# Kernel tuning notes

Hardware: AMD Instinct MI355X
Metric: run time of the kernel (lower is better)

## Reference

```python
import jax, jax.numpy as jnp
import numpy as np

B, L, D, H = 4, 4096, 1024, 4
DK = D // H          # per-head dim, d_k == d_v == 256
C = 64               # chunk size for chunked delta rule
NC = L // C
KS = 4               # short-conv kernel size
EPS = 1e-5           # norm_eps


def _silu(x):
    return x * jax.nn.sigmoid(x)


def _l2norm(x):
    return x * jax.lax.rsqrt((x * x).sum(-1, keepdims=True) + 1e-6)


def _depthwise_conv(x, w):
    # x: [b, l, d], w: [d, ks]. torch Conv1d(groups=d, padding=ks//2) then trim to l
    # == asymmetric padding (ks//2, ks//2 - 1) giving exactly length l.
    xt = jnp.swapaxes(x, 1, 2)  # [b, d, l]
    out = jax.lax.conv_general_dilated(
        xt, w[:, None, :], window_strides=(1,), padding=[(KS // 2, KS // 2 - 1)],
        feature_group_count=x.shape[-1], dimension_numbers=('NCH', 'OIH', 'NCH'))
    return jnp.swapaxes(out, 1, 2)


def setup_inputs() -> dict:
    key = jax.random.key(0)
    ks = jax.random.split(key, 16)
    nrm = lambda k, shp, s: jax.random.normal(k, shp, jnp.float32) * s
    s = 0.02
    FH = DK // 2
    return {
        'x': nrm(ks[0], (B, L, D), 1.0),
        'Wq': nrm(ks[1], (D, D), s), 'Wk': nrm(ks[2], (D, D), s), 'Wv': nrm(ks[3], (D, D), s),
        'Wb': nrm(ks[4], (D, H), s), 'Wg': nrm(ks[5], (D, D), s), 'Wo': nrm(ks[6], (D, D), s),
        'cq': nrm(ks[7], (D, KS), 0.2), 'ck': nrm(ks[8], (D, KS), 0.2), 'cv': nrm(ks[9], (D, KS), 0.2),
        'Wbil': nrm(ks[10], (H, DK, DK), 0.1 / np.sqrt(DK)),
        'temp': jnp.full((H,), float(np.sqrt(DK)), jnp.float32),
        'fw1': nrm(ks[11], (2 * DK + 1, FH), s), 'fb1': jnp.zeros((FH,), jnp.float32),
        'fw2': nrm(ks[12], (FH, 1), s), 'fb2': jnp.zeros((1,), jnp.float32),
        'rms_w': jnp.ones((DK,), jnp.float32),
        'lam_fast': jnp.full((H,), 0.3, jnp.float32),
        'lam_slow': jnp.full((H,), 0.9, jnp.float32),
    }


def reference(x, Wq, Wk, Wv, Wb, Wg, Wo, cq, ck, cv, Wbil, temp,
              fw1, fb1, fw2, fb2, rms_w, lam_fast, lam_slow):
    b, l, d = x.shape
    h, dk = H, DK

    # projections + depthwise short convolution + silu (qk_activation='silu')
    q = _silu(_depthwise_conv(x @ Wq, cq))
    k = _silu(_depthwise_conv(x @ Wk, ck))
    v = _silu(_depthwise_conv(x @ Wv, cv))
    beta = jax.nn.sigmoid(x @ Wb)                      # [b, l, h]

    def to_chunks(t):
        # [b, l, h*dk] -> [b, h, nc, C, dk]
        return t.reshape(b, NC, C, h, dk).transpose(0, 3, 1, 2, 4)

    q = _l2norm(to_chunks(q))                          # qk_norm='l2'
    k = _l2norm(to_chunks(k))
    v = to_chunks(v)
    beta = beta.reshape(b, NC, C, h).transpose(0, 3, 1, 2)  # [b,h,nc,C]

    k_beta = k * beta[..., None]
    v_beta = v * beta[..., None]

    strict = jnp.tril(jnp.ones((C, C), x.dtype), -1)
    causal = jnp.tril(jnp.ones((C, C), x.dtype))

    # intra-chunk delta-rule solve: T = (I + strictly_lower(k_beta k^T))^-1
    A = jnp.einsum('bhncd,bhned->bhnce', k_beta, k) * strict
    T = jnp.linalg.inv(jnp.eye(C, dtype=x.dtype) + A)
    w = jnp.einsum('bhnce,bhned->bhncd', T, k_beta)    # [b,h,nc,C,dk]
    u = jnp.einsum('bhnce,bhned->bhncd', T, v_beta)    # [b,h,nc,C,dv]

    # chunk-level bilinear resonance flux (vectorized 5-dim branch)
    k_proj = jnp.einsum('bhnck,hkv->bhncv', k, Wbil)
    avg_attn = (k_proj * u).sum(-1).mean(-1) / temp[None, :, None]   # [b,h,nc]
    flux_in = jnp.concatenate([k.mean(3), u.mean(3), avg_attn[..., None]], -1)
    h1 = _silu(flux_in @ fw1 + fb1)
    psi = jnp.clip(jax.nn.sigmoid(h1 @ fw2 + fb2)[..., 0], 0.01, 0.99)  # [b,h,nc]

    # chunk-sequential scan with hierarchical dual-state memory
    qs = jnp.moveaxis(q, 2, 0)
    ks_ = jnp.moveaxis(k, 2, 0)
    ws = jnp.moveaxis(w, 2, 0)
    us = jnp.moveaxis(u, 2, 0)
    psis = jnp.moveaxis(psi, 2, 0)                     # [nc,b,h]
    S0 = jnp.zeros((b, h, dk, dk), x.dtype)
    lf = lam_fast[None, :, None, None]
    ls = lam_slow[None, :, None, None]

    def step(carry, inp):
        Sf, Ss = carry
        qc, kc, wc, uc, pc = inp
        S = Sf + Ss
        u_i = uc - jnp.einsum('bhcd,bhdv->bhcv', wc, S)
        attn = jnp.einsum('bhcd,bhed->bhce', qc, kc) * causal
        o = jnp.einsum('bhcd,bhdv->bhcv', qc, S) + jnp.einsum('bhce,bhev->bhcv', attn, u_i)
        dS = jnp.einsum('bhcd,bhcv->bhdv', kc, u_i)
        p = pc[..., None, None]
        Sf = lf * Sf + p * dS
        Ss = ls * Ss + (1.0 - p) * dS
        return (Sf, Ss), o

    _, o = jax.lax.scan(step, (S0, S0), (qs, ks_, ws, us, psis))
    o = o.transpose(1, 0, 3, 2, 4).reshape(b, l, h, dk)  # [b,l,h,dv]

    # gated RMSNorm (FusedRMSNormGated, per-head)
    g = (x @ Wg).reshape(b, l, h, dk)
    o = o * jax.lax.rsqrt((o * o).mean(-1, keepdims=True) + EPS) * rms_w * jax.nn.sigmoid(g)
    return o.reshape(b, l, d) @ Wo
```

## Files before the change

kernel.cpp:

```cpp
#include <hip/hip_runtime.h>
#include <hip/hip_bf16.h>
#include <type_traits>
#include <stdint.h>

typedef __hip_bfloat16 bf16;
typedef unsigned short u16t;


__device__ __forceinline__ float sigmoidf_(float x) { return 1.0f / (1.0f + __expf(-x)); }

__device__ __forceinline__ float bu2f(unsigned short u) {
    return __uint_as_float(((unsigned)u) << 16);
}
__device__ __forceinline__ float2 bu2f2(const unsigned short* p) {
    ushort2 t = *(const ushort2*)p;
    float2 r; r.x = bu2f(t.x); r.y = bu2f(t.y); return r;
}
__device__ __forceinline__ float4 ld4(const float* p) { return *(const float4*)p; }
__device__ __forceinline__ float4 ld4(const bf16* p) {
    ushort4 u = *(const ushort4*)p;
    float4 r;
    r.x = bu2f(u.x); r.y = bu2f(u.y); r.z = bu2f(u.z); r.w = bu2f(u.w);
    return r;
}
__device__ __forceinline__ unsigned short f2bu(float x) {
    bf16 h = __float2bfloat16(x);
    return *reinterpret_cast<unsigned short*>(&h);
}
__device__ __forceinline__ void st4(bf16* p, float a, float b, float c, float d) {
    ushort4 u = { f2bu(a), f2bu(b), f2bu(c), f2bu(d) };
    *(ushort4*)p = u;
}
__device__ __forceinline__ float b2f(bf16 h) { return __bfloat162float(h); }

typedef __bf16 bfv8 __attribute__((ext_vector_type(8)));
typedef float f32x4v __attribute__((ext_vector_type(4)));

__device__ __forceinline__ void gl_lds16(const bf16* g, bf16* l) {
    __builtin_amdgcn_global_load_lds(
        (const __attribute__((address_space(1))) unsigned int*)g,
        (__attribute__((address_space(3))) unsigned int*)l,
        16, 0, 0);
}

template <typename OutT>
__global__ __launch_bounds__(256)
void mfma_gemm(const bf16* __restrict__ A, const bf16* __restrict__ Bt,
               OutT* __restrict__ Cm, int M, int N, int K,
               size_t aStride, size_t bStride, size_t cStride, int hMask)
{
    __shared__ __align__(16) bf16 As[4096];
    __shared__ __align__(16) bf16 Bs[4096];
    const int z = blockIdx.z;
    A  += (size_t)z * aStride;
    Bt += (size_t)(z & hMask) * bStride;
    Cm += (size_t)z * cStride;
    const int tid = threadIdx.x;
    const int wid = tid >> 6, lane = tid & 63;
    const int nwg = gridDim.x * gridDim.y;
    int bid = blockIdx.y * gridDim.x + blockIdx.x;
    bid = (bid & 7) * (nwg >> 3) + (bid >> 3);
    const int bx = bid % gridDim.x, by = bid / gridDim.x;
    const int m0 = by << 7, n0 = bx << 7;
    const int wr = wid >> 1, wc = wid & 1;

    const int srow = tid >> 2;
    const int scol = (tid & 3) << 3;
    const bf16* agp = A  + (size_t)(m0 + srow) * K + scol;
    const bf16* bgp = Bt + (size_t)(n0 + srow) * K + scol;
    const size_t rowskip = (size_t)64 * K;
    bf16* al0 = As + wid * 512;
    bf16* al1 = As + 2048 + wid * 512;
    bf16* bl0 = Bs + wid * 512;
    bf16* bl1 = Bs + 2048 + wid * 512;

    const int aoff = (wr * 64 + (lane & 15)) * 32 + ((lane >> 4) << 3);
    const int boff = (wc * 64 + (lane & 15)) * 32 + ((lane >> 4) << 3);

    const f32x4v vzero = {0.f, 0.f, 0.f, 0.f};
    f32x4v acc[4][4];
#pragma unroll
    for (int i = 0; i < 4; ++i)
#pragma unroll
        for (int j = 0; j < 4; ++j) acc[i][j] = vzero;

    for (int k0 = 0; k0 < K; k0 += 32) {
        gl_lds16(agp,           al0);
        gl_lds16(agp + rowskip, al1);
        gl_lds16(bgp,           bl0);
        gl_lds16(bgp + rowskip, bl1);
        agp += 32; bgp += 32;
        __syncthreads();
        bfv8 af[4], bfr[4];
#pragma unroll
        for (int i = 0; i < 4; ++i) {
            af[i]  = *(const bfv8*)(As + aoff + i * 16 * 32);
            bfr[i] = *(const bfv8*)(Bs + boff + i * 16 * 32);
        }
#pragma unroll
        for (int mi = 0; mi < 4; ++mi)
#pragma unroll
            for (int ni = 0; ni < 4; ++ni)
                acc[mi][ni] = __builtin_amdgcn_mfma_f32_16x16x32_bf16(
                    af[mi], bfr[ni], acc[mi][ni], 0, 0, 0);
        __syncthreads();
    }

    const int crow = (lane >> 4) << 2;
    const int ccol = lane & 15;
#pragma unroll
    for (int mi = 0; mi < 4; ++mi)
#pragma unroll
        for (int ni = 0; ni < 4; ++ni)
#pragma unroll
            for (int j = 0; j < 4; ++j) {
                size_t r = (size_t)(m0 + wr * 64 + mi * 16 + crow + j) * N
                         + (n0 + wc * 64 + ni * 16 + ccol);
                if constexpr (std::is_same<OutT, float>::value)
                    Cm[r] = acc[mi][ni][j];
                else
                    Cm[r] = __float2bfloat16(acc[mi][ni][j]);
            }
}

__global__ __launch_bounds__(256)
void castx_kernel(const float* __restrict__ x, bf16* __restrict__ xb)
{
    size_t i = ((size_t)blockIdx.x * 256 + threadIdx.x) * 8;
    float4 a = ld4(&x[i]);
    float4 b = ld4(&x[i + 4]);
    st4(xb + i,     a.x, a.y, a.z, a.w);
    st4(xb + i + 4, b.x, b.y, b.z, b.w);
}

__global__ __launch_bounds__(256)
void castT_kernel(const float* __restrict__ W, bf16* __restrict__ Wt)
{
    __shared__ float tile[32][33];
    const int tid = threadIdx.x;
    const int tx = tid & 31, ty = tid >> 5;
    const int c0 = blockIdx.x << 5, r0 = blockIdx.y << 5;
#pragma unroll
    for (int r = 0; r < 4; ++r)
        tile[ty + r * 8][tx] = W[(size_t)(r0 + ty + r * 8) * 1024 + c0 + tx];
    __syncthreads();
#pragma unroll
    for (int r = 0; r < 4; ++r)
        Wt[(size_t)(c0 + ty + r * 8) * 1024 + r0 + tx] =
            __float2bfloat16(tile[tx][ty + r * 8]);
}

__global__ __launch_bounds__(256)
void castTb_kernel(const float* __restrict__ W, bf16* __restrict__ Wt)
{
    __shared__ float tile[32][33];
    const int tid = threadIdx.x;
    const int tx = tid & 31, ty = tid >> 5;
    const int c0 = blockIdx.x << 5, r0 = blockIdx.y << 5;
    const size_t hb = (size_t)blockIdx.z << 16;
#pragma unroll
    for (int r = 0; r < 4; ++r)
        tile[ty + r * 8][tx] = W[hb + (size_t)(r0 + ty + r * 8) * 256 + c0 + tx];
    __syncthreads();
#pragma unroll
    for (int r = 0; r < 4; ++r)
        Wt[hb + (size_t)(c0 + ty + r * 8) * 256 + r0 + tx] =
            __float2bfloat16(tile[tx][ty + r * 8]);
}

__global__ __launch_bounds__(256)
void conv_kernel(const bf16* __restrict__ xin, const float* __restrict__ cw,
                 bf16* __restrict__ outc, int doNorm)
{
    const int bt = blockIdx.x;
    const int b = bt >> 12, t = bt & 4095;
    const int tid = threadIdx.x;
    const int h = tid >> 6, lane = tid & 63;
    const int i0 = lane << 2;
    const int d = (h << 8) + i0;
    float w0[4], w1[4], w2[4], w3[4];
    {
        float4 c0 = *(const float4*)&cw[(d + 0) * 4];
        float4 c1 = *(const float4*)&cw[(d + 1) * 4];
        float4 c2 = *(const float4*)&cw[(d + 2) * 4];
        float4 c3 = *(const float4*)&cw[(d + 3) * 4];
        w0[0] = c0.x; w0[1] = c0.y; w0[2] = c0.z; w0[3] = c0.w;
        w1[0] = c1.x; w1[1] = c1.y; w1[2] = c1.z; w1[3] = c1.w;
        w2[0] = c2.x; w2[1] = c2.y; w2[2] = c2.z; w2[3] = c2.w;
        w3[0] = c3.x; w3[1] = c3.y; w3[2] = c3.z; w3[3] = c3.w;
    }
    float acc[4] = {0.f, 0.f, 0.f, 0.f};
#pragma unroll
    for (int jj = 0; jj < 4; ++jj) {
        int tt = t - 2 + jj;
        if (tt >= 0 && tt < 4096) {
            float4 xr = ld4(&xin[((size_t)(b << 12) + tt) * 1024 + d]);
            acc[0] += xr.x * w0[jj];
            acc[1] += xr.y * w1[jj];
            acc[2] += xr.z * w2[jj];
            acc[3] += xr.w * w3[jj];
        }
    }
#pragma unroll
    for (int j = 0; j < 4; ++j) acc[j] *= sigmoidf_(acc[j]);
    if (doNorm) {
        float ss = acc[0]*acc[0] + acc[1]*acc[1] + acc[2]*acc[2] + acc[3]*acc[3];
#pragma unroll
        for (int off = 32; off > 0; off >>= 1) ss += __shfl_xor(ss, off);
        float r = rsqrtf(ss + 1e-6f);
        acc[0] *= r; acc[1] *= r; acc[2] *= r; acc[3] *= r;
    }
    st4(&outc[(((size_t)((b << 2) + h)) * 4096 + t) * 256 + i0],
        acc[0], acc[1], acc[2], acc[3]);
}

__global__ __launch_bounds__(256)
void beta_kernel(const float* __restrict__ x, const float* __restrict__ Wb,
                 float* __restrict__ beta)
{
    const int bt = blockIdx.x;
    const int b = bt >> 12, t = bt & 4095;
    const int tid = threadIdx.x;
    const int wv = tid >> 6;
    __shared__ float redB[4][4];
    float4 xv = *(const float4*)&x[(size_t)bt * 1024 + (tid << 2)];
    float xa[4] = {xv.x, xv.y, xv.z, xv.w};
    float a[4] = {0.f, 0.f, 0.f, 0.f};
#pragma unroll
    for (int j = 0; j < 4; ++j) {
        float4 wr = *(const float4*)&Wb[((tid << 2) + j) * 4];
        a[0] += xa[j] * wr.x; a[1] += xa[j] * wr.y;
        a[2] += xa[j] * wr.z; a[3] += xa[j] * wr.w;
    }
#pragma unroll
    for (int hh = 0; hh < 4; ++hh)
#pragma unroll
        for (int off = 32; off > 0; off >>= 1) a[hh] += __shfl_xor(a[hh], off);
    if ((tid & 63) == 0) {
        redB[wv][0] = a[0]; redB[wv][1] = a[1]; redB[wv][2] = a[2]; redB[wv][3] = a[3];
    }
    __syncthreads();
    if (tid < 4) {
        float s = redB[0][tid] + redB[1][tid] + redB[2][tid] + redB[3][tid];
        beta[((size_t)((b << 2) + tid)) * 4096 + t] = sigmoidf_(s);
    }
}

#define AST 68
__global__ __launch_bounds__(256)
void chunk_kernel(const bf16* kG, const bf16* vG,
                  const bf16* qG, const float* betaG,
                  const bf16* kprojG,
                  const float* fw1, const float* fb1,
                  const float* fw2, const float* fb2,
                  const float* tempG,
                  bf16* uOut, bf16* wOut,
                  bf16* attnOut, float* psiOut)
{
    __shared__ __align__(16) u16t kLs[64 * 256];
    __shared__ __align__(16) float Abuf[64 * AST];
    __shared__ float betaL[64];
    __shared__ float fluxL[648];
    __shared__ float redL[256];

    const int chunk = blockIdx.x;
    const int bh = chunk >> 6;
    const int n  = chunk & 63;
    const int h  = bh & 3;
    const int tid = threadIdx.x;
    const int wv = tid >> 6, l = tid & 63;
    const int l15 = l & 15, l4 = l >> 4;
    const size_t base = ((size_t)bh * 4096 + n * 64) * 256;
    const u16t* kg = (const u16t*)kG;
    const u16t* qg = (const u16t*)qG;
    const f32x4v vz = {0.f, 0.f, 0.f, 0.f};

#pragma unroll
    for (int r = 0; r < 8; ++r) {
        int idx = r * 256 + tid;
        int c = idx >> 5, d0 = (idx & 31) << 3;
        ulonglong2 t16 = *(const ulonglong2*)&kg[base + c * 256 + d0];
        *(ulonglong2*)&kLs[c * 256 + (d0 ^ ((c & 7) << 3))] = t16;
    }
    if (tid < 64) betaL[tid] = betaG[(size_t)bh * 4096 + (n << 6) + tid];
    __syncthreads();

    {
        const int arow = (wv << 4) + l15;
        const int kc = l4 << 3;
        f32x4v accA[4] = {vz, vz, vz, vz};
#pragma unroll
        for (int ks = 0; ks < 8; ++ks) {
            const int dbase = (ks << 5) + kc;
            bfv8 afr = *(const bfv8*)&kLs[arow * 256 + (dbase ^ ((arow & 7) << 3))];
#pragma unroll
            for (int et = 0; et < 4; ++et) {
                const int brow = (et << 4) + l15;
                bfv8 bfr = *(const bfv8*)&kLs[brow * 256 + (dbase ^ ((brow & 7) << 3))];
                accA[et] = __builtin_amdgcn_mfma_f32_16x16x32_bf16(afr, bfr, accA[et], 0, 0, 0);
            }
        }
#pragma unroll
        for (int j = 0; j < 4; ++j) {
            const int c = (wv << 4) + (l4 << 2) + j;
            const float bc = betaL[c];
#pragma unroll
            for (int et = 0; et < 4; ++et) {
                const int e = (et << 4) + l15;
                Abuf[c * AST + e] = (e < c) ? accA[et][j] * bc : 0.f;
            }
        }
    }
    __syncthreads();

    float ur[64], wr_[64];
#pragma unroll
    for (int c = 0; c < 64; ++c) {
        ur[c]  = betaL[c] * b2f(vG[base + c * 256 + tid]);
        wr_[c] = betaL[c] * bu2f(kLs[c * 256 + (tid ^ ((c & 7) << 3))]);
    }
#pragma unroll
    for (int c = 1; c < 64; ++c) {
        float sU = 0.f, sW = 0.f;
        const int G = (c + 3) >> 2;
#pragma unroll
        for (int g = 0; g < G; ++g) {
            float4 a4 = *(const float4*)&Abuf[c * AST + (g << 2)];
            sU += a4.x * ur[(g << 2) + 0] + a4.y * ur[(g << 2) + 1]
                + a4.z * ur[(g << 2) + 2] + a4.w * ur[(g << 2) + 3];
            sW += a4.x * wr_[(g << 2) + 0] + a4.y * wr_[(g << 2) + 1]
                + a4.z * wr_[(g << 2) + 2] + a4.w * wr_[(g << 2) + 3];
        }
        ur[c] -= sU;
        wr_[c] -= sW;
    }

    float um = 0.f, accv = 0.f, km = 0.f;
#pragma unroll
    for (int c = 0; c < 64; ++c) {
        uOut[base + c * 256 + tid] = __float2bfloat16(ur[c]);
        um += ur[c];
        accv += b2f(kprojG[base + c * 256 + tid]) * ur[c];
        km += bu2f(kLs[c * 256 + (tid ^ ((c & 7) << 3))]);
    }
#pragma unroll
    for (int c = 0; c < 64; ++c)
        wOut[base + c * 256 + tid] = __float2bfloat16(wr_[c]);

    fluxL[tid]       = km * (1.f / 64.f);
    fluxL[256 + tid] = um * (1.f / 64.f);
    redL[tid] = accv;
    __syncthreads();
    for (int s2 = 128; s2 > 0; s2 >>= 1) {
        if (tid < s2) redL[tid] += redL[tid + s2];
        __syncthreads();
    }
    if (tid == 0) fluxL[512] = redL[0] * (1.f / 64.f) / tempG[h];
    __syncthreads();
    {
        float a = 0.f;
        if (tid < 128) {
            for (int i2 = 0; i2 < 256; ++i2) a += fluxL[i2] * fw1[i2 * 128 + tid];
        } else {
            const int j = tid - 128;
            for (int i2 = 256; i2 < 513; ++i2) a += fluxL[i2] * fw1[i2 * 128 + j];
        }
        redL[tid] = a;
    }
    __syncthreads();
    if (tid < 128) {
        float a = fb1[tid] + redL[tid] + redL[tid + 128];
        a *= sigmoidf_(a);
        fluxL[520 + tid] = a;
    }
    __syncthreads();
    if (tid < 64) {
        float p = fluxL[520 + tid] * fw2[tid] + fluxL[520 + 64 + tid] * fw2[64 + tid];
#pragma unroll
        for (int off = 32; off > 0; off >>= 1) p += __shfl_xor(p, off);
        if (tid == 0) {
            float ps = sigmoidf_(p + fb2[0]);
            psiOut[chunk] = fminf(0.99f, fmaxf(0.01f, ps));
        }
    }

    u16t* qLs = (u16t*)Abuf;
    const size_t abase = (size_t)chunk << 12;
    const int ct = wv >> 1, e0 = (wv & 1) << 1;
    const int qrow = (ct << 4) + l15;
    const int kc = l4 << 3;
    for (int hh = 0; hh < 2; ++hh) {
        __syncthreads();
#pragma unroll
        for (int r = 0; r < 4; ++r) {
            int idx = r * 256 + tid;
            int rr = idx >> 5, d0 = (idx & 31) << 3;
            ulonglong2 t16 = *(const ulonglong2*)&qg[base + (size_t)((hh << 5) + rr) * 256 + d0];
            *(ulonglong2*)&qLs[rr * 256 + (d0 ^ ((rr & 7) << 3))] = t16;
        }
        __syncthreads();
        f32x4v accQ[2] = {vz, vz};
#pragma unroll
        for (int ks = 0; ks < 8; ++ks) {
            const int dbase = (ks << 5) + kc;
            bfv8 qfr = *(const bfv8*)&qLs[qrow * 256 + (dbase ^ ((qrow & 7) << 3))];
#pragma unroll
            for (int ep = 0; ep < 2; ++ep) {
                const int brow = ((e0 + ep) << 4) + l15;
                bfv8 bfr = *(const bfv8*)&kLs[brow * 256 + (dbase ^ ((brow & 7) << 3))];
                accQ[ep] = __builtin_amdgcn_mfma_f32_16x16x32_bf16(qfr, bfr, accQ[ep], 0, 0, 0);
            }
        }
#pragma unroll
        for (int j = 0; j < 4; ++j) {
            const int c = (hh << 5) + (ct << 4) + (l4 << 2) + j;
#pragma unroll
            for (int ep = 0; ep < 2; ++ep) {
                const int e = ((e0 + ep) << 4) + l15;
                attnOut[abase + c * 64 + e] = __float2bfloat16((e <= c) ? accQ[ep][j] : 0.f);
            }
        }
    }
}

#define KTS 260
__global__ __launch_bounds__(256)
void ktr_kernel(bf16* kG)
{
    __shared__ u16t tile[64 * KTS];
    const size_t base = (size_t)blockIdx.x << 14;
    const int tid = threadIdx.x;
    u16t* kg = (u16t*)kG;
#pragma unroll
    for (int r = 0; r < 16; ++r) {
        int e4 = r * 256 + tid;
        int c = e4 >> 6, dd = (e4 & 63) << 2;
        ushort4 t4 = *(const ushort4*)&kg[base + c * 256 + dd];
        *(ushort4*)&tile[c * KTS + dd] = t4;
    }
    __syncthreads();
#pragma unroll
    for (int r = 0; r < 16; ++r) {
        int e4 = r * 256 + tid;
        int d = e4 >> 4, cc = (e4 & 15) << 2;
        ushort4 o4;
        o4.x = tile[(cc + 0) * KTS + d];
        o4.y = tile[(cc + 1) * KTS + d];
        o4.z = tile[(cc + 2) * KTS + d];
        o4.w = tile[(cc + 3) * KTS + d];
        *(ushort4*)&kg[base + d * 64 + cc] = o4;
    }
}

__global__ __launch_bounds__(256, 1)
void scan_kernel(const bf16* __restrict__ qG, const bf16* __restrict__ kTG,
                 const bf16* __restrict__ wG, const bf16* __restrict__ uG,
                 const bf16* __restrict__ attnG, const float* __restrict__ psiG,
                 const float* __restrict__ lamF, const float* __restrict__ lamS,
                 bf16* __restrict__ oG)
{
    __shared__ __align__(16) u16t ssumT[16 * 256];
    __shared__ __align__(16) u16t uiT[16 * 64];

    const int bidx = blockIdx.x;
    const int bh = bidx >> 4, vb = bidx & 15;
    const int h = bh & 3;
    const int v0 = vb << 4;
    const int tid = threadIdx.x;
    const int wv = tid >> 6, l = tid & 63;
    const int l15 = l & 15, l4 = l >> 4;
    const float lf = lamF[h], ls = lamS[h];

    const int cA   = (wv << 4) + l15;
    const int cO   = (wv << 4) + (l4 << 2);
    const int kcol = l4 << 3;
    const int sw15 = (l15 & 7) << 3;

    const f32x4v vzero = {0.f, 0.f, 0.f, 0.f};
    f32x4v Sf[4], Ss[4];
#pragma unroll
    for (int t = 0; t < 4; ++t) { Sf[t] = vzero; Ss[t] = vzero; }

    const size_t bhbase = (size_t)bh * 4096 * 256;

    for (int n = 0; n < 64; ++n) {
        const size_t base = bhbase + ((size_t)n << 14);
        const size_t ab = (size_t)((bh << 6) + n) << 12;
        const float p = psiG[(bh << 6) + n];

#pragma unroll
        for (int t = 0; t < 4; ++t) {
            const int d = (((wv << 2) + t) << 4) + l15;
            f32x4v sv = Sf[t] + Ss[t];
#pragma unroll
            for (int j = 0; j < 4; ++j) {
                const int v = (l4 << 2) + j;
                ssumT[v * 256 + (d ^ ((v & 7) << 3))] = f2bu(sv[j]);
            }
        }
        bfv8 wA[8], qA[8], aA[2], kB[4][2];
#pragma unroll
        for (int ks = 0; ks < 8; ++ks) {
            wA[ks] = *(const bfv8*)&wG[base + (size_t)cA * 256 + (ks << 5) + kcol];
            qA[ks] = *(const bfv8*)&qG[base + (size_t)cA * 256 + (ks << 5) + kcol];
        }
#pragma unroll
        for (int ks = 0; ks < 2; ++ks)
            aA[ks] = *(const bfv8*)&attnG[ab + cA * 64 + (ks << 5) + kcol];
#pragma unroll
        for (int t = 0; t < 4; ++t) {
            const int d = (((wv << 2) + t) << 4) + l15;
            kB[t][0] = *(const bfv8*)&kTG[base + d * 64 + kcol];
            kB[t][1] = *(const bfv8*)&kTG[base + d * 64 + 32 + kcol];
        }
        float u4[4];
#pragma unroll
        for (int j = 0; j < 4; ++j)
            u4[j] = b2f(uG[base + (size_t)(cO + j) * 256 + v0 + l15]);
        __syncthreads();

        bfv8 sB[8];
#pragma unroll
        for (int ks = 0; ks < 8; ++ks)
            sB[ks] = *(const bfv8*)&ssumT[l15 * 256 + (((ks << 5) + kcol) ^ sw15)];
        f32x4v T = vzero;
#pragma unroll
        for (int ks = 0; ks < 8; ++ks)
            T = __builtin_amdgcn_mfma_f32_16x16x32_bf16(wA[ks], sB[ks], T, 0, 0, 0);
        {
            ushort4 uw;
            uw.x = f2bu(u4[0] - T[0]); uw.y = f2bu(u4[1] - T[1]);
            uw.z = f2bu(u4[2] - T[2]); uw.w = f2bu(u4[3] - T[3]);
            *(ushort4*)&uiT[l15 * 64 + (cO ^ sw15)] = uw;
        }
        __syncthreads();

        bfv8 uT[2];
        uT[0] = *(const bfv8*)&uiT[l15 * 64 + (kcol ^ sw15)];
        uT[1] = *(const bfv8*)&uiT[l15 * 64 + ((32 + kcol) ^ sw15)];
        f32x4v oa = vzero;
        oa = __builtin_amdgcn_mfma_f32_16x16x32_bf16(aA[0], uT[0], oa, 0, 0, 0);
        oa = __builtin_amdgcn_mfma_f32_16x16x32_bf16(aA[1], uT[1], oa, 0, 0, 0);
#pragma unroll
        for (int ks = 0; ks < 8; ++ks)
            oa = __builtin_amdgcn_mfma_f32_16x16x32_bf16(qA[ks], sB[ks], oa, 0, 0, 0);
#pragma unroll
        for (int j = 0; j < 4; ++j)
            oG[base + (size_t)(cO + j) * 256 + v0 + l15] = __float2bfloat16(oa[j]);
        const float pn = 1.f - p;
#pragma unroll
        for (int t = 0; t < 4; ++t) {
            f32x4v ds = vzero;
            ds = __builtin_amdgcn_mfma_f32_16x16x32_bf16(uT[0], kB[t][0], ds, 0, 0, 0);
            ds = __builtin_amdgcn_mfma_f32_16x16x32_bf16(uT[1], kB[t][1], ds, 0, 0, 0);
            Sf[t] = lf * Sf[t] + p  * ds;
            Ss[t] = ls * Ss[t] + pn * ds;
        }
    }
}

__global__ __launch_bounds__(256)
void fnorm_kernel(const bf16* __restrict__ oS, const bf16* __restrict__ xg,
                  const float* __restrict__ rmsw, bf16* __restrict__ outn)
{
    const int bt = blockIdx.x;
    const int b = bt >> 12, t = bt & 4095;
    const int tid = threadIdx.x;
    const int h = tid >> 6, lane = tid & 63;
    const int i0 = lane << 2;
    float4 o4 = ld4(&oS[(((size_t)((b << 2) + h)) * 4096 + t) * 256 + i0]);
    float ss = o4.x * o4.x + o4.y * o4.y + o4.z * o4.z + o4.w * o4.w;
#pragma unroll
    for (int off = 32; off > 0; off >>= 1) ss += __shfl_xor(ss, off);
    float r = rsqrtf(ss * (1.f / 256.f) + 1e-5f);
    float4 g4 = ld4(&xg[(size_t)bt * 1024 + (h << 8) + i0]);
    float4 w4 = *(const float4*)&rmsw[i0];
    st4(&outn[(size_t)bt * 1024 + (h << 8) + i0],
        o4.x * r * w4.x * sigmoidf_(g4.x),
        o4.y * r * w4.y * sigmoidf_(g4.y),
        o4.z * r * w4.z * sigmoidf_(g4.z),
        o4.w * r * w4.w * sigmoidf_(g4.w));
}

extern "C" void kernel_launch(void* const* d_in, const int* in_sizes, int n_in,
                              void* d_out, int out_size, void* d_ws, size_t ws_size,
                              hipStream_t stream)
{
    const float* x    = (const float*)d_in[0];
    const float* Wq   = (const float*)d_in[1];
    const float* Wk   = (const float*)d_in[2];
    const float* Wv   = (const float*)d_in[3];
    const float* Wb   = (const float*)d_in[4];
    const float* Wg   = (const float*)d_in[5];
    const float* Wo   = (const float*)d_in[6];
    const float* cq   = (const float*)d_in[7];
    const float* ck   = (const float*)d_in[8];
    const float* cv   = (const float*)d_in[9];
    const float* Wbil = (const float*)d_in[10];
    const float* temp = (const float*)d_in[11];
    const float* fw1  = (const float*)d_in[12];
    const float* fb1  = (const float*)d_in[13];
    const float* fw2  = (const float*)d_in[14];
    const float* fb2  = (const float*)d_in[15];
    const float* rmsw = (const float*)d_in[16];
    const float* lamF = (const float*)d_in[17];
    const float* lamS = (const float*)d_in[18];
    float* out = (float*)d_out;

    const size_t SZ = 16777216ull;
    bf16* bws = (bf16*)d_ws;
    bf16* S0 = bws;
    bf16* S1 = bws + SZ;
    bf16* S2 = bws + 2 * SZ;
    bf16* S3 = bws + 3 * SZ;
    bf16* S4 = bws + 4 * SZ;
    bf16* S5 = bws + 5 * SZ;
    bf16* attnB = bws + 6 * SZ;
    float* p_beta = (float*)(bws + 6 * SZ + 4194304);
    float* p_psi  = p_beta + 65536;

    bf16* Wqt = attnB;
    bf16* Wkt = attnB + 1048576;
    bf16* Wvt = attnB + 2097152;
    bf16* Wgt = attnB + 3145728;

    castx_kernel<<<8192, 256, 0, stream>>>(x, S5);
    castT_kernel<<<dim3(32, 32), 256, 0, stream>>>(Wq, Wqt);
    castT_kernel<<<dim3(32, 32), 256, 0, stream>>>(Wk, Wkt);
    castT_kernel<<<dim3(32, 32), 256, 0, stream>>>(Wv, Wvt);
    castT_kernel<<<dim3(32, 32), 256, 0, stream>>>(Wg, Wgt);

    dim3 gM(8, 128);
    mfma_gemm<bf16><<<gM, 256, 0, stream>>>(S5, Wqt, S0, 16384, 1024, 1024, 0, 0, 0, 0);
    conv_kernel<<<16384, 256, 0, stream>>>(S0, cq, S1, 1);
    mfma_gemm<bf16><<<gM, 256, 0, stream>>>(S5, Wkt, S0, 16384, 1024, 1024, 0, 0, 0, 0);
    conv_kernel<<<16384, 256, 0, stream>>>(S0, ck, S2, 1);
    mfma_gemm<bf16><<<gM, 256, 0, stream>>>(S5, Wvt, S0, 16384, 1024, 1024, 0, 0, 0, 0);
    conv_kernel<<<16384, 256, 0, stream>>>(S0, cv, S3, 0);
    mfma_gemm<bf16><<<gM, 256, 0, stream>>>(S5, Wgt, S0, 16384, 1024, 1024, 0, 0, 0, 0);
    beta_kernel<<<16384, 256, 0, stream>>>(x, Wb, p_beta);

    bf16* Wbilt = attnB;
    castTb_kernel<<<dim3(8, 8, 4), 256, 0, stream>>>(Wbil, Wbilt);
    mfma_gemm<bf16><<<dim3(2, 32, 16), 256, 0, stream>>>(
        S2, Wbilt, S4, 4096, 256, 256, 1048576ull, 65536ull, 1048576ull, 3);
    chunk_kernel<<<1024, 256, 0, stream>>>(
        S2, S3, S1, p_beta, S4, fw1, fb1, fw2, fb2, temp,
        S5 , S4 , attnB, p_psi);
    ktr_kernel<<<1024, 256, 0, stream>>>(S2);
    scan_kernel<<<256, 256, 0, stream>>>(
        S1, S2, S4, S5, attnB, p_psi, lamF, lamS, S3 );
    castT_kernel<<<dim3(32, 32), 256, 0, stream>>>(Wo, attnB);
    fnorm_kernel<<<16384, 256, 0, stream>>>(S3, S0, rmsw, S1);
    mfma_gemm<float><<<gM, 256, 0, stream>>>(S1, attnB, out, 16384, 1024, 1024, 0, 0, 0, 0);
}
```

Before: 1.150 ms.

## Double chunk_kernel threads, splitting u and w triangular solves across halves

The chunk kernel goes from 256 to 512 threads. The first half runs the forward substitution for u and the second half for w, so each thread holds one 64-float array instead of two. The MFMA tiles, the loads and the fw1 reduction are redistributed over 8 waves. This targets register pressure and serial per-thread work, which limit occupancy and latency in the per-chunk solve. The cost is more threads per block and more reduction and synchronisation traffic.

Result: faster. 1.017 ms (-11.5%).

```diff
diff --git a/kernel.cpp b/kernel.cpp
--- a/kernel.cpp
+++ b/kernel.cpp
@@ -247,7 +247,7 @@
 }
 
 #define AST 68
-__global__ __launch_bounds__(256)
+__global__ __launch_bounds__(512)
 void chunk_kernel(const bf16* kG, const bf16* vG,
                   const bf16* qG, const float* betaG,
                   const bf16* kprojG,
@@ -261,7 +261,7 @@
     __shared__ __align__(16) float Abuf[64 * AST];
     __shared__ float betaL[64];
     __shared__ float fluxL[648];
-    __shared__ float redL[256];
+    __shared__ float redL[512];
 
     const int chunk = blockIdx.x;
     const int bh = chunk >> 6;
@@ -276,8 +276,8 @@
     const f32x4v vz = {0.f, 0.f, 0.f, 0.f};
 
 #pragma unroll
-    for (int r = 0; r < 8; ++r) {
-        int idx = r * 256 + tid;
+    for (int r = 0; r < 4; ++r) {
+        int idx = r * 512 + tid;
         int c = idx >> 5, d0 = (idx & 31) << 3;
         ulonglong2 t16 = *(const ulonglong2*)&kg[base + c * 256 + d0];
         *(ulonglong2*)&kLs[c * 256 + (d0 ^ ((c & 7) << 3))] = t16;
@@ -286,71 +286,82 @@
     __syncthreads();
 
     {
-        const int arow = (wv << 4) + l15;
+        const int rb = wv >> 1, cp = wv & 1;
+        const int arow = (rb << 4) + l15;
         const int kc = l4 << 3;
-        f32x4v accA[4] = {vz, vz, vz, vz};
+        f32x4v accA[2] = {vz, vz};
 #pragma unroll
         for (int ks = 0; ks < 8; ++ks) {
             const int dbase = (ks << 5) + kc;
             bfv8 afr = *(const bfv8*)&kLs[arow * 256 + (dbase ^ ((arow & 7) << 3))];
 #pragma unroll
-            for (int et = 0; et < 4; ++et) {
-                const int brow = (et << 4) + l15;
+            for (int et = 0; et < 2; ++et) {
+                const int brow = ((cp * 2 + et) << 4) + l15;
                 bfv8 bfr = *(const bfv8*)&kLs[brow * 256 + (dbase ^ ((brow & 7) << 3))];
                 accA[et] = __builtin_amdgcn_mfma_f32_16x16x32_bf16(afr, bfr, accA[et], 0, 0, 0);
             }
         }
 #pragma unroll
         for (int j = 0; j < 4; ++j) {
-            const int c = (wv << 4) + (l4 << 2) + j;
+            const int c = (rb << 4) + (l4 << 2) + j;
             const float bc = betaL[c];
 #pragma unroll
-            for (int et = 0; et < 4; ++et) {
-                const int e = (et << 4) + l15;
+            for (int et = 0; et < 2; ++et) {
+                const int e = ((cp * 2 + et) << 4) + l15;
                 Abuf[c * AST + e] = (e < c) ? accA[et][j] * bc : 0.f;
             }
         }
     }
     __syncthreads();
 
-    float ur[64], wr_[64];
-#pragma unroll
-    for (int c = 0; c < 64; ++c) {
-        ur[c]  = betaL[c] * b2f(vG[base + c * 256 + tid]);
-        wr_[c] = betaL[c] * bu2f(kLs[c * 256 + (tid ^ ((c & 7) << 3))]);
+    const int half = tid >> 8;
+    const int ts = tid & 255;
+    float st[64];
+    float km = 0.f;
+    if (half == 0) {
+#pragma unroll
+        for (int c = 0; c < 64; ++c)
+            st[c] = betaL[c] * b2f(vG[base + c * 256 + ts]);
+    } else {
+#pragma unroll
+        for (int c = 0; c < 64; ++c) {
+            float kv = bu2f(kLs[c * 256 + (ts ^ ((c & 7) << 3))]);
+            km += kv;
+            st[c] = betaL[c] * kv;
+        }
     }
 #pragma unroll
     for (int c = 1; c < 64; ++c) {
-        float sU = 0.f, sW = 0.f;
+        float s = 0.f;
         const int G = (c + 3) >> 2;
 #pragma unroll
         for (int g = 0; g < G; ++g) {
             float4 a4 = *(const float4*)&Abuf[c * AST + (g << 2)];
-            sU += a4.x * ur[(g << 2) + 0] + a4.y * ur[(g << 2) + 1]
-                + a4.z * ur[(g << 2) + 2] + a4.w * ur[(g << 2) + 3];
-            sW += a4.x * wr_[(g << 2) + 0] + a4.y * wr_[(g << 2) + 1]
-                + a4.z * wr_[(g << 2) + 2] + a4.w * wr_[(g << 2) + 3];
-        }
-        ur[c] -= sU;
-        wr_[c] -= sW;
-    }
-
-    float um = 0.f, accv = 0.f, km = 0.f;
-#pragma unroll
-    for (int c = 0; c < 64; ++c) {
-        uOut[base + c * 256 + tid] = __float2bfloat16(ur[c]);
-        um += ur[c];
-        accv += b2f(kprojG[base + c * 256 + tid]) * ur[c];
-        km += bu2f(kLs[c * 256 + (tid ^ ((c & 7) << 3))]);
-    }
-#pragma unroll
-    for (int c = 0; c < 64; ++c)
-        wOut[base + c * 256 + tid] = __float2bfloat16(wr_[c]);
-
-    fluxL[tid]       = km * (1.f / 64.f);
-    fluxL[256 + tid] = um * (1.f / 64.f);
-    redL[tid] = accv;
-    __syncthreads();
+            s += a4.x * st[(g << 2) + 0] + a4.y * st[(g << 2) + 1]
+               + a4.z * st[(g << 2) + 2] + a4.w * st[(g << 2) + 3];
+        }
+        st[c] -= s;
+    }
+
+    if (half == 0) {
+        float um = 0.f, accv = 0.f;
+#pragma unroll
+        for (int c = 0; c < 64; ++c) {
+            uOut[base + c * 256 + ts] = __float2bfloat16(st[c]);
+            um += st[c];
+            accv += b2f(kprojG[base + c * 256 + ts]) * st[c];
+        }
+        fluxL[256 + ts] = um * (1.f / 64.f);
+        redL[ts] = accv;
+    } else {
+        fluxL[ts] = km * (1.f / 64.f);
+    }
+    __syncthreads();
+    if (half == 1) {
+#pragma unroll
+        for (int c = 0; c < 64; ++c)
+            wOut[base + c * 256 + ts] = __float2bfloat16(st[c]);
+    }
     for (int s2 = 128; s2 > 0; s2 >>= 1) {
         if (tid < s2) redL[tid] += redL[tid + s2];
         __syncthreads();
@@ -358,18 +369,16 @@
     if (tid == 0) fluxL[512] = redL[0] * (1.f / 64.f) / tempG[h];
     __syncthreads();
     {
+        const int g = tid >> 7, j = tid & 127;
+        const int i0 = g << 7;
+        const int i1 = (g == 3) ? 513 : (i0 + 128);
         float a = 0.f;
-        if (tid < 128) {
-            for (int i2 = 0; i2 < 256; ++i2) a += fluxL[i2] * fw1[i2 * 128 + tid];
-        } else {
-            const int j = tid - 128;
-            for (int i2 = 256; i2 < 513; ++i2) a += fluxL[i2] * fw1[i2 * 128 + j];
-        }
+        for (int i2 = i0; i2 < i1; ++i2) a += fluxL[i2] * fw1[i2 * 128 + j];
         redL[tid] = a;
     }
     __syncthreads();
     if (tid < 128) {
-        float a = fb1[tid] + redL[tid] + redL[tid + 128];
+        float a = fb1[tid] + redL[tid] + redL[128 + tid] + redL[256 + tid] + redL[384 + tid];
         a *= sigmoidf_(a);
         fluxL[520 + tid] = a;
     }
@@ -386,39 +395,33 @@
 
     u16t* qLs = (u16t*)Abuf;
     const size_t abase = (size_t)chunk << 12;
-    const int ct = wv >> 1, e0 = (wv & 1) << 1;
-    const int qrow = (ct << 4) + l15;
+    const int ct2 = wv >> 2, eq = wv & 3;
+    const int qrow = (ct2 << 4) + l15;
     const int kc = l4 << 3;
     for (int hh = 0; hh < 2; ++hh) {
         __syncthreads();
 #pragma unroll
-        for (int r = 0; r < 4; ++r) {
-            int idx = r * 256 + tid;
+        for (int r = 0; r < 2; ++r) {
+            int idx = r * 512 + tid;
             int rr = idx >> 5, d0 = (idx & 31) << 3;
             ulonglong2 t16 = *(const ulonglong2*)&qg[base + (size_t)((hh << 5) + rr) * 256 + d0];
             *(ulonglong2*)&qLs[rr * 256 + (d0 ^ ((rr & 7) << 3))] = t16;
         }
         __syncthreads();
-        f32x4v accQ[2] = {vz, vz};
+        f32x4v accQ = vz;
 #pragma unroll
         for (int ks = 0; ks < 8; ++ks) {
             const int dbase = (ks << 5) + kc;
             bfv8 qfr = *(const bfv8*)&qLs[qrow * 256 + (dbase ^ ((qrow & 7) << 3))];
-#pragma unroll
-            for (int ep = 0; ep < 2; ++ep) {
-                const int brow = ((e0 + ep) << 4) + l15;
-                bfv8 bfr = *(const bfv8*)&kLs[brow * 256 + (dbase ^ ((brow & 7) << 3))];
-                accQ[ep] = __builtin_amdgcn_mfma_f32_16x16x32_bf16(qfr, bfr, accQ[ep], 0, 0, 0);
-            }
+            const int brow = (eq << 4) + l15;
+            bfv8 bfr = *(const bfv8*)&kLs[brow * 256 + (dbase ^ ((brow & 7) << 3))];
+            accQ = __builtin_amdgcn_mfma_f32_16x16x32_bf16(qfr, bfr, accQ, 0, 0, 0);
         }
 #pragma unroll
         for (int j = 0; j < 4; ++j) {
-            const int c = (hh << 5) + (ct << 4) + (l4 << 2) + j;
-#pragma unroll
-            for (int ep = 0; ep < 2; ++ep) {
-                const int e = ((e0 + ep) << 4) + l15;
-                attnOut[abase + c * 64 + e] = __float2bfloat16((e <= c) ? accQ[ep][j] : 0.f);
-            }
+            const int c = (hh << 5) + (ct2 << 4) + (l4 << 2) + j;
+            const int e = (eq << 4) + l15;
+            attnOut[abase + c * 64 + e] = __float2bfloat16((e <= c) ? accQ[j] : 0.f);
         }
     }
 }
@@ -644,7 +647,7 @@
     castTb_kernel<<<dim3(8, 8, 4), 256, 0, stream>>>(Wbil, Wbilt);
     mfma_gemm<bf16><<<dim3(2, 32, 16), 256, 0, stream>>>(
         S2, Wbilt, S4, 4096, 256, 256, 1048576ull, 65536ull, 1048576ull, 3);
-    chunk_kernel<<<1024, 256, 0, stream>>>(
+    chunk_kernel<<<1024, 512, 0, stream>>>(
         S2, S3, S1, p_beta, S4, fw1, fb1, fw2, fb2, temp,
         S5 , S4 , attnB, p_psi);
     ktr_kernel<<<1024, 256, 0, stream>>>(S2);
```
